# Optimization experiments

Hardware: AMD Instinct MI355X
Metric: run time of the kernel (lower is better)

Reference implementation:

```python
import math
import jax, jax.numpy as jnp
import numpy as np

B, N, C = 2, 2048, 1024
H = 16
D = C // H  # 64
LN_EPS = 1e-5


def setup_inputs() -> dict:
    key = jax.random.key(0)
    ks = jax.random.split(key, 5)
    x = jax.random.normal(ks[0], (B, N, C), dtype=jnp.float32)
    w_qkv = jax.random.normal(ks[1], (C, 3 * C), dtype=jnp.float32) * 0.02
    w_proj = jax.random.normal(ks[2], (C, C), dtype=jnp.float32) * 0.02
    b_proj = jnp.zeros((C,), dtype=jnp.float32)
    ln_w = jnp.ones((D,), dtype=jnp.float32) + jax.random.normal(ks[3], (D,), dtype=jnp.float32) * 0.02
    ln_b = jax.random.normal(ks[4], (D,), dtype=jnp.float32) * 0.02
    return {"x": x, "w_qkv": w_qkv, "w_proj": w_proj, "b_proj": b_proj,
            "ln_w": ln_w, "ln_b": ln_b}


def _layernorm(t, w, b):
    mu = jnp.mean(t, axis=-1, keepdims=True)
    var = jnp.var(t, axis=-1, keepdims=True)
    return (t - mu) * jax.lax.rsqrt(var + LN_EPS) * w + b


def reference(x, w_qkv, w_proj, b_proj, ln_w, ln_b):
    b, n, c = x.shape
    h, d = H, c // H
    # QKV projection (no bias): [b,n,3c] -> [3,b,h,n,d]
    qkv = (x @ w_qkv).reshape(b, n, 3, h, d).transpose(2, 0, 3, 1, 4)
    q, k, v = qkv[0], qkv[1], qkv[2]
    # per-head LayerNorm on q and k (qk_norm)
    q = _layernorm(q, ln_w, ln_b)
    k = _layernorm(k, ln_w, ln_b)
    # NOTE: source multiplies q by sqrt(head_dim) (faithful to original)
    q = q * jnp.asarray(math.sqrt(d), dtype=q.dtype)
    scores = jnp.einsum('bhnd,bhmd->bhnm', q, k)  # [b,h,n,n]
    mask_value = -jnp.finfo(scores.dtype).max
    causal = jnp.tril(jnp.ones((n, n), dtype=bool))
    scores = jnp.where(causal, scores, mask_value)
    attn = jax.nn.softmax(scores, axis=-1)
    out = jnp.einsum('bhnm,bhmd->bhnd', attn, v)  # [b,h,n,d]
    out = out.transpose(0, 2, 1, 3).reshape(b, n, c)  # b n (h d)
    return out @ w_proj + b_proj
```

## Files before the change

kernel.cpp:

```cpp
#include <hip/hip_runtime.h>

#define LOG2E 1.4426950408889634f

typedef _Float16 f16x8_t __attribute__((ext_vector_type(8)));
typedef _Float16 f16x4_t __attribute__((ext_vector_type(4)));
typedef float    f32x4_t __attribute__((ext_vector_type(4)));

__device__ __forceinline__ void async_copy16(void* lds, const void* g) {
    __builtin_amdgcn_global_load_lds(
        (const __attribute__((address_space(1))) unsigned char*)g,
        (__attribute__((address_space(3))) unsigned char*)lds, 16, 0, 0);
}

__global__ void cast_f32_f16_k(const float* __restrict__ in, _Float16* __restrict__ out, int n4) {
    int i = blockIdx.x * blockDim.x + threadIdx.x;
    if (i >= n4) return;
    float4 v = ((const float4*)in)[i];
    f16x4_t o = { (_Float16)v.x, (_Float16)v.y, (_Float16)v.z, (_Float16)v.w };
    ((f16x4_t*)out)[i] = o;
}

__global__ void transpose_cast_k(const float* __restrict__ in, _Float16* __restrict__ out,
                                 int R, int C) {
    __shared__ _Float16 tl[64][65];
    const int t = threadIdx.x;
    const int c = t & 63;
    const int r4 = t >> 6;
    const int r0 = blockIdx.y * 64, c0 = blockIdx.x * 64;
#pragma unroll
    for (int i = 0; i < 16; ++i) {
        int r = r4 + i * 4;
        tl[c][r] = (_Float16)in[(size_t)(r0 + r) * C + c0 + c];
    }
    __syncthreads();
#pragma unroll
    for (int i = 0; i < 16; ++i) {
        int rr = r4 + i * 4;
        out[(size_t)(c0 + rr) * R + r0 + c] = tl[rr][c];
    }
}

template <typename OutT, bool BIAS>
__global__ __launch_bounds__(256, 2)
void gemm_f16_k(const _Float16* __restrict__ A, const _Float16* __restrict__ BT,
                OutT* __restrict__ C, const float* __restrict__ bias,
                int M, int N, int K) {
    __shared__ _Float16 As[2][128][32];
    __shared__ _Float16 Bs[2][128][32];
    const int tid = threadIdx.x;
    const int wid = tid >> 6, lane = tid & 63;
    const int qd = lane >> 4, ln = lane & 15;
    const int m0 = blockIdx.x * 128, n0 = blockIdx.y * 128;
    const int wm = (wid >> 1) * 64, wn = (wid & 1) * 64;

    f32x4_t acc[4][4] = {};

    const int srow = lane >> 2;
    const int skk  = (lane & 3) * 8;

    for (int k0 = 0; k0 < K; k0 += 64) {
        __syncthreads();
#pragma unroll
        for (int p = 0; p < 4; ++p) {
            const int seg = p * 4 + wid;
            const int s   = seg >> 3;
            const int rg  = seg & 7;
            const int row = rg * 16 + srow;
            const size_t goff = (size_t)row * K + k0 + s * 32 + skk;
            async_copy16(&As[0][0][0] + seg * 512, A  + (size_t)m0 * K + goff);
            async_copy16(&Bs[0][0][0] + seg * 512, BT + (size_t)n0 * K + goff);
        }
        __syncthreads();
#pragma unroll
        for (int s = 0; s < 2; ++s) {
            f16x8_t a[4], b[4];
#pragma unroll
            for (int i = 0; i < 4; ++i)
                a[i] = *(const f16x8_t*)&As[s][wm + i * 16 + ln][qd * 8];
#pragma unroll
            for (int j = 0; j < 4; ++j)
                b[j] = *(const f16x8_t*)&Bs[s][wn + j * 16 + ln][qd * 8];
#pragma unroll
            for (int i = 0; i < 4; ++i)
#pragma unroll
                for (int j = 0; j < 4; ++j)
                    acc[i][j] = __builtin_amdgcn_mfma_f32_16x16x32_f16(a[i], b[j], acc[i][j], 0, 0, 0);
        }
    }
#pragma unroll
    for (int i = 0; i < 4; ++i)
#pragma unroll
        for (int j = 0; j < 4; ++j) {
            const int col = n0 + wn + j * 16 + ln;
            const float bv = BIAS ? bias[col] : 0.0f;
#pragma unroll
            for (int r = 0; r < 4; ++r) {
                const int row = m0 + wm + i * 16 + qd * 4 + r;
                C[(size_t)row * N + col] = (OutT)(acc[i][j][r] + bv);
            }
        }
}

__global__ void ln_qkv_k(const _Float16* __restrict__ qkv, const float* __restrict__ ln_w,
                         const float* __restrict__ ln_b, _Float16* __restrict__ Qb,
                         _Float16* __restrict__ Kb, _Float16* __restrict__ Vb) {
    const int tid = threadIdx.x;
    const int wid = tid >> 6, lane = tid & 63;
    const int row = blockIdx.x * 4 + wid;
    const int t = row >> 4;
    const int h = row & 15;
    const int b = t >> 11, n = t & 2047;
    const size_t base = (size_t)t * 3072 + h * 64 + lane;
    float q = (float)qkv[base];
    float k = (float)qkv[base + 1024];
    float v = (float)qkv[base + 2048];
    const float wv = ln_w[lane], bv = ln_b[lane];

    float sq = q, sk = k;
#pragma unroll
    for (int m = 1; m < 64; m <<= 1) { sq += __shfl_xor(sq, m); sk += __shfl_xor(sk, m); }
    sq *= (1.0f / 64.0f); sk *= (1.0f / 64.0f);
    const float dq = q - sq, dk = k - sk;
    float vq = dq * dq, vk = dk * dk;
#pragma unroll
    for (int m = 1; m < 64; m <<= 1) { vq += __shfl_xor(vq, m); vk += __shfl_xor(vk, m); }
    vq *= (1.0f / 64.0f); vk *= (1.0f / 64.0f);
    const float yq = dq * rsqrtf(vq + 1e-5f) * wv + bv;
    const float yk = dk * rsqrtf(vk + 1e-5f) * wv + bv;
    const size_t obase = ((size_t)((b * 16 + h) * 2048 + n)) * 64 + lane;
    Qb[obase] = (_Float16)(yq * (8.0f * LOG2E));
    Kb[obase] = (_Float16)yk;
    Vb[obase] = (_Float16)v;
}

__global__ __launch_bounds__(256, 2)
void attn_k(const _Float16* __restrict__ Q, const _Float16* __restrict__ K,
            const _Float16* __restrict__ V, _Float16* __restrict__ O) {
    __shared__ _Float16 Ks[2][64][32];
    __shared__ _Float16 VT[64][72];
    __shared__ _Float16 Pl[4][16][72];

    const int tid = threadIdx.x;
    const int wid = tid >> 6, lane = tid & 63;
    const int qd = lane >> 4, ln = lane & 15;
    const int bh = blockIdx.x;
    const int band = 31 - blockIdx.y;
    const int b = bh >> 4, h = bh & 15;
    const size_t kvbase = (size_t)bh * 2048 * 64;
    const int qrow0 = band * 64 + wid * 16;

    f16x8_t qf[2];
#pragma unroll
    for (int s = 0; s < 2; ++s)
        qf[s] = *(const f16x8_t*)&Q[kvbase + (size_t)(qrow0 + ln) * 64 + s * 32 + qd * 8];

    const f16x8_t ones = { (_Float16)1.f, (_Float16)1.f, (_Float16)1.f, (_Float16)1.f,
                           (_Float16)1.f, (_Float16)1.f, (_Float16)1.f, (_Float16)1.f };

    f32x4_t o[4] = {};
    f32x4_t ol = {};
    float mr[4] = { -3.0e38f, -3.0e38f, -3.0e38f, -3.0e38f };

    const int nsteps = band + 1;

    for (int st = 0; st < nsteps; ++st) {
        const int kv0 = st * 64;
        __syncthreads();
#pragma unroll
        for (int p = 0; p < 2; ++p) {
            const int seg = p * 4 + wid;
            const int oh = seg * 512;
            const int hidx = oh + lane * 8;
            const int s_ = hidx >> 11;
            const int rrow = (hidx >> 5) & 63;
            const int kk = hidx & 31;
            async_copy16((_Float16*)Ks + oh,
                         K + kvbase + (size_t)(kv0 + rrow) * 64 + s_ * 32 + kk);
        }
#pragma unroll
        for (int e = 0; e < 2; ++e) {
            const int idx = tid + e * 256;
            const int kv = idx & 63;
            const int d0 = (idx >> 6) * 8;
            f16x8_t vv = *(const f16x8_t*)&V[kvbase + (size_t)(kv0 + kv) * 64 + d0];
#pragma unroll
            for (int j = 0; j < 8; ++j) VT[d0 + j][kv] = vv[j];
        }
        __syncthreads();

        f32x4_t sc[4];
#pragma unroll
        for (int j = 0; j < 4; ++j) {
            f16x8_t kb0 = *(const f16x8_t*)&Ks[0][j * 16 + ln][qd * 8];
            f16x8_t kb1 = *(const f16x8_t*)&Ks[1][j * 16 + ln][qd * 8];
            f32x4_t s0 = {};
            s0 = __builtin_amdgcn_mfma_f32_16x16x32_f16(qf[0], kb0, s0, 0, 0, 0);
            s0 = __builtin_amdgcn_mfma_f32_16x16x32_f16(qf[1], kb1, s0, 0, 0, 0);
            sc[j] = s0;
        }
        if (st == nsteps - 1) {
#pragma unroll
            for (int j = 0; j < 4; ++j) {
                const int kv = kv0 + j * 16 + ln;
#pragma unroll
                for (int r = 0; r < 4; ++r) {
                    const int qr = qrow0 + qd * 4 + r;
                    if (kv > qr) sc[j][r] = -3.0e38f;
                }
            }
        }
#pragma unroll
        for (int r = 0; r < 4; ++r) {
            float mx = fmaxf(fmaxf(sc[0][r], sc[1][r]), fmaxf(sc[2][r], sc[3][r]));
            mx = fmaxf(mx, __shfl_xor(mx, 1));
            mx = fmaxf(mx, __shfl_xor(mx, 2));
            mx = fmaxf(mx, __shfl_xor(mx, 4));
            mx = fmaxf(mx, __shfl_xor(mx, 8));
            const float mn = fmaxf(mr[r], mx);
            const float al = exp2f(mr[r] - mn);
            mr[r] = mn;
            const int prow = qd * 4 + r;
#pragma unroll
            for (int j = 0; j < 4; ++j) {
                const float p = exp2f(sc[j][r] - mn);
                Pl[wid][prow][j * 16 + ln] = (_Float16)p;
            }
#pragma unroll
            for (int dt = 0; dt < 4; ++dt) o[dt][r] *= al;
            ol[r] *= al;
        }
        asm volatile("s_waitcnt lgkmcnt(0)" ::: "memory");
        f16x8_t p0 = *(const f16x8_t*)&Pl[wid][ln][qd * 8];
        f16x8_t p1 = *(const f16x8_t*)&Pl[wid][ln][32 + qd * 8];
#pragma unroll
        for (int dt = 0; dt < 4; ++dt) {
            f16x8_t v0 = *(const f16x8_t*)&VT[dt * 16 + ln][qd * 8];
            f16x8_t v1 = *(const f16x8_t*)&VT[dt * 16 + ln][32 + qd * 8];
            o[dt] = __builtin_amdgcn_mfma_f32_16x16x32_f16(p0, v0, o[dt], 0, 0, 0);
            o[dt] = __builtin_amdgcn_mfma_f32_16x16x32_f16(p1, v1, o[dt], 0, 0, 0);
        }
        ol = __builtin_amdgcn_mfma_f32_16x16x32_f16(p0, ones, ol, 0, 0, 0);
        ol = __builtin_amdgcn_mfma_f32_16x16x32_f16(p1, ones, ol, 0, 0, 0);
    }
#pragma unroll
    for (int r = 0; r < 4; ++r) {
        const float inv = 1.0f / ol[r];
        const int qr = qrow0 + qd * 4 + r;
#pragma unroll
        for (int dt = 0; dt < 4; ++dt)
            O[((size_t)(b * 2048 + qr)) * 1024 + h * 64 + dt * 16 + ln] =
                (_Float16)(o[dt][r] * inv);
    }
}

extern "C" void kernel_launch(void* const* d_in, const int* in_sizes, int n_in,
                              void* d_out, int out_size, void* d_ws, size_t ws_size,
                              hipStream_t stream) {
    const float* x      = (const float*)d_in[0];
    const float* w_qkv  = (const float*)d_in[1];
    const float* w_proj = (const float*)d_in[2];
    const float* b_proj = (const float*)d_in[3];
    const float* ln_w   = (const float*)d_in[4];
    const float* ln_b   = (const float*)d_in[5];
    float* out = (float*)d_out;

    char* w = (char*)d_ws;
    _Float16*  qkv    = (_Float16*)w;  w += (size_t)4096 * 3072 * 2;
    _Float16*  xh     = (_Float16*)w;  w += (size_t)4096 * 1024 * 2;
    _Float16*  wqkvT  = (_Float16*)w;  w += (size_t)3072 * 1024 * 2;
    _Float16*  wprojT = (_Float16*)w;  w += (size_t)1024 * 1024 * 2;
    _Float16*  Qb     = (_Float16*)w;  w += (size_t)32 * 2048 * 64 * 2;
    _Float16*  Kb     = (_Float16*)w;  w += (size_t)32 * 2048 * 64 * 2;
    _Float16*  Vb     = (_Float16*)w;  w += (size_t)32 * 2048 * 64 * 2;
    _Float16*  Ah     = (_Float16*)w;  w += (size_t)4096 * 1024 * 2;

    cast_f32_f16_k<<<4096, 256, 0, stream>>>(x, xh, 4096 * 1024 / 4);
    transpose_cast_k<<<dim3(48, 16), 256, 0, stream>>>(w_qkv, wqkvT, 1024, 3072);
    transpose_cast_k<<<dim3(16, 16), 256, 0, stream>>>(w_proj, wprojT, 1024, 1024);
    gemm_f16_k<_Float16, false><<<dim3(32, 24), 256, 0, stream>>>(xh, wqkvT, qkv, nullptr, 4096, 3072, 1024);
    ln_qkv_k<<<16384, 256, 0, stream>>>(qkv, ln_w, ln_b, Qb, Kb, Vb);
    attn_k<<<dim3(32, 32), 256, 0, stream>>>(Qb, Kb, Vb, Ah);
    gemm_f16_k<float, true><<<dim3(32, 8), 256, 0, stream>>>(Ah, wprojT, out, b_proj, 4096, 1024, 1024);
}
```

Baseline: 220.3 us.

## Pair causal query bands per block and keep P in registers

Each attention block now handles a high and a low query band (hib = 31-lob), so every block does the same total amount of causal work and reuses each K/V tile loaded into LDS for both bands. The grid drops from 32x32 to 32x16. Scores are computed transposed (K as the A operand), which lets the probabilities feed the PV MFMA (16x16x16) straight from registers, removing the P round-trip through LDS and the extra MFMA against a ones vector for the row sum. The V transpose in LDS uses an XOR swizzle to avoid bank conflicts, in exchange for more register pressure and more, smaller MFMAs.

```diff
diff --git a/kernel.cpp b/kernel.cpp
--- a/kernel.cpp
+++ b/kernel.cpp
@@ -5,6 +5,9 @@
 typedef _Float16 f16x8_t __attribute__((ext_vector_type(8)));
 typedef _Float16 f16x4_t __attribute__((ext_vector_type(4)));
 typedef float    f32x4_t __attribute__((ext_vector_type(4)));
+
+#define MFMA32(a, b, c) __builtin_amdgcn_mfma_f32_16x16x32_f16(a, b, c, 0, 0, 0)
+#define MFMA16(a, b, c) __builtin_amdgcn_mfma_f32_16x16x16f16(a, b, c, 0, 0, 0)
 
 __device__ __forceinline__ void async_copy16(void* lds, const void* g) {
     __builtin_amdgcn_global_load_lds(
@@ -84,7 +87,7 @@
             for (int i = 0; i < 4; ++i)
 #pragma unroll
                 for (int j = 0; j < 4; ++j)
-                    acc[i][j] = __builtin_amdgcn_mfma_f32_16x16x32_f16(a[i], b[j], acc[i][j], 0, 0, 0);
+                    acc[i][j] = MFMA32(a[i], b[j], acc[i][j]);
         }
     }
 #pragma unroll
@@ -137,44 +140,44 @@
 void attn_k(const _Float16* __restrict__ Q, const _Float16* __restrict__ K,
             const _Float16* __restrict__ V, _Float16* __restrict__ O) {
     __shared__ _Float16 Ks[2][64][32];
-    __shared__ _Float16 VT[64][72];
-    __shared__ _Float16 Pl[4][16][72];
+    __shared__ _Float16 VT[64][64];
 
     const int tid = threadIdx.x;
     const int wid = tid >> 6, lane = tid & 63;
     const int qd = lane >> 4, ln = lane & 15;
     const int bh = blockIdx.x;
-    const int band = 31 - blockIdx.y;
     const int b = bh >> 4, h = bh & 15;
+    const int lob = blockIdx.y;
+    const int hib = 31 - lob;
     const size_t kvbase = (size_t)bh * 2048 * 64;
-    const int qrow0 = band * 64 + wid * 16;
-
-    f16x8_t qf[2];
-#pragma unroll
-    for (int s = 0; s < 2; ++s)
-        qf[s] = *(const f16x8_t*)&Q[kvbase + (size_t)(qrow0 + ln) * 64 + s * 32 + qd * 8];
-
-    const f16x8_t ones = { (_Float16)1.f, (_Float16)1.f, (_Float16)1.f, (_Float16)1.f,
-                           (_Float16)1.f, (_Float16)1.f, (_Float16)1.f, (_Float16)1.f };
-
-    f32x4_t o[4] = {};
-    f32x4_t ol = {};
-    float mr[4] = { -3.0e38f, -3.0e38f, -3.0e38f, -3.0e38f };
-
-    const int nsteps = band + 1;
-
-    for (int st = 0; st < nsteps; ++st) {
+    const int qh0 = hib * 64 + wid * 16;
+    const int ql0 = lob * 64 + wid * 16;
+
+    f16x8_t qfh[2], qfl[2];
+#pragma unroll
+    for (int s = 0; s < 2; ++s) {
+        qfh[s] = *(const f16x8_t*)&Q[kvbase + (size_t)(qh0 + ln) * 64 + s * 32 + qd * 8];
+        qfl[s] = *(const f16x8_t*)&Q[kvbase + (size_t)(ql0 + ln) * 64 + s * 32 + qd * 8];
+    }
+
+    f32x4_t oh[4] = {}, olo[4] = {};
+    float mh = -3.0e38f, ml = -3.0e38f;
+    float lh = 0.0f, ll = 0.0f;
+
+    const int nst = hib + 1;
+
+    for (int st = 0; st < nst; ++st) {
         const int kv0 = st * 64;
         __syncthreads();
 #pragma unroll
         for (int p = 0; p < 2; ++p) {
             const int seg = p * 4 + wid;
-            const int oh = seg * 512;
-            const int hidx = oh + lane * 8;
+            const int oh_ = seg * 512;
+            const int hidx = oh_ + lane * 8;
             const int s_ = hidx >> 11;
             const int rrow = (hidx >> 5) & 63;
             const int kk = hidx & 31;
-            async_copy16((_Float16*)Ks + oh,
+            async_copy16((_Float16*)Ks + oh_,
                          K + kvbase + (size_t)(kv0 + rrow) * 64 + s_ * 32 + kk);
         }
 #pragma unroll
@@ -184,73 +187,94 @@
             const int d0 = (idx >> 6) * 8;
             f16x8_t vv = *(const f16x8_t*)&V[kvbase + (size_t)(kv0 + kv) * 64 + d0];
 #pragma unroll
-            for (int j = 0; j < 8; ++j) VT[d0 + j][kv] = vv[j];
+            for (int j = 0; j < 8; ++j) {
+                const int d = d0 + j;
+                const int col = (((kv >> 2) ^ (d & 15)) << 2) | (kv & 3);
+                VT[d][col] = vv[j];
+            }
         }
         __syncthreads();
 
-        f32x4_t sc[4];
-#pragma unroll
-        for (int j = 0; j < 4; ++j) {
-            f16x8_t kb0 = *(const f16x8_t*)&Ks[0][j * 16 + ln][qd * 8];
-            f16x8_t kb1 = *(const f16x8_t*)&Ks[1][j * 16 + ln][qd * 8];
-            f32x4_t s0 = {};
-            s0 = __builtin_amdgcn_mfma_f32_16x16x32_f16(qf[0], kb0, s0, 0, 0, 0);
-            s0 = __builtin_amdgcn_mfma_f32_16x16x32_f16(qf[1], kb1, s0, 0, 0, 0);
-            sc[j] = s0;
-        }
-        if (st == nsteps - 1) {
-#pragma unroll
-            for (int j = 0; j < 4; ++j) {
-                const int kv = kv0 + j * 16 + ln;
+        f16x8_t kb[4][2];
+#pragma unroll
+        for (int jt = 0; jt < 4; ++jt)
+#pragma unroll
+            for (int s = 0; s < 2; ++s)
+                kb[jt][s] = *(const f16x8_t*)&Ks[s][jt * 16 + ln][qd * 8];
+        f16x4_t vf[4][4];
+#pragma unroll
+        for (int dt = 0; dt < 4; ++dt)
+#pragma unroll
+            for (int c = 0; c < 4; ++c)
+                vf[dt][c] = *(const f16x4_t*)&VT[dt * 16 + ln][(((c * 4 + qd) ^ ln) << 2)];
+
+        auto process = [&](const f16x8_t (&qf)[2], f32x4_t (&o)[4], float& m, float& l,
+                           int q0w, bool diag) {
+            f32x4_t sc[4];
+#pragma unroll
+            for (int jt = 0; jt < 4; ++jt) {
+                f32x4_t s = {};
+                s = MFMA32(kb[jt][0], qf[0], s);
+                s = MFMA32(kb[jt][1], qf[1], s);
+                sc[jt] = s;
+            }
+            if (diag) {
+                const int qq = q0w + ln;
+#pragma unroll
+                for (int c = 0; c < 4; ++c)
+#pragma unroll
+                    for (int r = 0; r < 4; ++r)
+                        if (kv0 + c * 16 + qd * 4 + r > qq) sc[c][r] = -3.0e38f;
+            }
+            float mx = sc[0][0];
+#pragma unroll
+            for (int c = 0; c < 4; ++c)
+#pragma unroll
+                for (int r = 0; r < 4; ++r) mx = fmaxf(mx, sc[c][r]);
+            mx = fmaxf(mx, __shfl_xor(mx, 16));
+            mx = fmaxf(mx, __shfl_xor(mx, 32));
+            const float mn = fmaxf(m, mx);
+            const float al = exp2f(m - mn);
+            m = mn;
+            float rs = 0.0f;
+            f16x4_t pf[4];
+#pragma unroll
+            for (int c = 0; c < 4; ++c)
 #pragma unroll
                 for (int r = 0; r < 4; ++r) {
-                    const int qr = qrow0 + qd * 4 + r;
-                    if (kv > qr) sc[j][r] = -3.0e38f;
+                    const float p = exp2f(sc[c][r] - mn);
+                    rs += p;
+                    pf[c][r] = (_Float16)p;
                 }
-            }
-        }
-#pragma unroll
-        for (int r = 0; r < 4; ++r) {
-            float mx = fmaxf(fmaxf(sc[0][r], sc[1][r]), fmaxf(sc[2][r], sc[3][r]));
-            mx = fmaxf(mx, __shfl_xor(mx, 1));
-            mx = fmaxf(mx, __shfl_xor(mx, 2));
-            mx = fmaxf(mx, __shfl_xor(mx, 4));
-            mx = fmaxf(mx, __shfl_xor(mx, 8));
-            const float mn = fmaxf(mr[r], mx);
-            const float al = exp2f(mr[r] - mn);
-            mr[r] = mn;
-            const int prow = qd * 4 + r;
-#pragma unroll
-            for (int j = 0; j < 4; ++j) {
-                const float p = exp2f(sc[j][r] - mn);
-                Pl[wid][prow][j * 16 + ln] = (_Float16)p;
-            }
-#pragma unroll
-            for (int dt = 0; dt < 4; ++dt) o[dt][r] *= al;
-            ol[r] *= al;
-        }
-        asm volatile("s_waitcnt lgkmcnt(0)" ::: "memory");
-        f16x8_t p0 = *(const f16x8_t*)&Pl[wid][ln][qd * 8];
-        f16x8_t p1 = *(const f16x8_t*)&Pl[wid][ln][32 + qd * 8];
+            l = l * al + rs;
+#pragma unroll
+            for (int dt = 0; dt < 4; ++dt) o[dt] *= al;
+#pragma unroll
+            for (int dt = 0; dt < 4; ++dt)
+#pragma unroll
+                for (int c = 0; c < 4; ++c)
+                    o[dt] = MFMA16(vf[dt][c], pf[c], o[dt]);
+        };
+
+        process(qfh, oh, mh, lh, qh0, st == hib);
+        if (st <= lob) process(qfl, olo, ml, ll, ql0, st == lob);
+    }
+
+    auto epi = [&](f32x4_t (&o)[4], float l, int q0w) {
+        float t = l + __shfl_xor(l, 16);
+        t = t + __shfl_xor(t, 32);
+        const float inv = 1.0f / t;
+        const size_t base = ((size_t)(b * 2048 + q0w + ln)) * 1024 + h * 64 + qd * 4;
 #pragma unroll
         for (int dt = 0; dt < 4; ++dt) {
-            f16x8_t v0 = *(const f16x8_t*)&VT[dt * 16 + ln][qd * 8];
-            f16x8_t v1 = *(const f16x8_t*)&VT[dt * 16 + ln][32 + qd * 8];
-            o[dt] = __builtin_amdgcn_mfma_f32_16x16x32_f16(p0, v0, o[dt], 0, 0, 0);
-            o[dt] = __builtin_amdgcn_mfma_f32_16x16x32_f16(p1, v1, o[dt], 0, 0, 0);
-        }
-        ol = __builtin_amdgcn_mfma_f32_16x16x32_f16(p0, ones, ol, 0, 0, 0);
-        ol = __builtin_amdgcn_mfma_f32_16x16x32_f16(p1, ones, ol, 0, 0, 0);
-    }
-#pragma unroll
-    for (int r = 0; r < 4; ++r) {
-        const float inv = 1.0f / ol[r];
-        const int qr = qrow0 + qd * 4 + r;
-#pragma unroll
-        for (int dt = 0; dt < 4; ++dt)
-            O[((size_t)(b * 2048 + qr)) * 1024 + h * 64 + dt * 16 + ln] =
-                (_Float16)(o[dt][r] * inv);
-    }
+            f16x4_t ov;
+#pragma unroll
+            for (int r = 0; r < 4; ++r) ov[r] = (_Float16)(o[dt][r] * inv);
+            *(f16x4_t*)&O[base + dt * 16] = ov;
+        }
+    };
+    epi(oh, lh, qh0);
+    epi(olo, ll, ql0);
 }
 
 extern "C" void kernel_launch(void* const* d_in, const int* in_sizes, int n_in,
@@ -279,6 +303,6 @@
     transpose_cast_k<<<dim3(16, 16), 256, 0, stream>>>(w_proj, wprojT, 1024, 1024);
     gemm_f16_k<_Float16, false><<<dim3(32, 24), 256, 0, stream>>>(xh, wqkvT, qkv, nullptr, 4096, 3072, 1024);
     ln_qkv_k<<<16384, 256, 0, stream>>>(qkv, ln_w, ln_b, Qb, Kb, Vb);
-    attn_k<<<dim3(32, 32), 256, 0, stream>>>(Qb, Kb, Vb, Ah);
+    attn_k<<<dim3(32, 16), 256, 0, stream>>>(Qb, Kb, Vb, Ah);
     gemm_f16_k<float, true><<<dim3(32, 8), 256, 0, stream>>>(Ah, wprojT, out, b_proj, 4096, 1024, 1024);
 }
```

Result: faster. 211.8 us (-3.8%).
